# Performance work log

Hardware: AMD Instinct MI355X
Metric: run time of the kernel (lower is better)

Reference implementation:

```python
import jax, jax.numpy as jnp
import numpy as np

H = 64          # hidden_dim
I = 4           # input_dim
L = 4           # num_layers
O = 5           # output_dim
B = 256         # batch
T = 2048        # seq_len


def setup_inputs() -> dict:
    key = jax.random.key(0)
    ks = jax.random.split(key, 20)
    s = 1.0 / np.sqrt(H)  # PyTorch GRU init scale
    x = jax.random.normal(ks[0], (B, T, I), dtype=jnp.float32)
    # layer 0 input->hidden weights ([3H, I]); layers 1..3 input is H
    w_ih0 = jax.random.uniform(ks[1], (3 * H, I), jnp.float32, -s, s)
    w_ih_rest = jax.random.uniform(ks[2], (L - 1, 3 * H, H), jnp.float32, -s, s)
    w_hh = jax.random.uniform(ks[3], (L, 3 * H, H), jnp.float32, -s, s)
    b_ih = jax.random.uniform(ks[4], (L, 3 * H), jnp.float32, -s, s)
    b_hh = jax.random.uniform(ks[5], (L, 3 * H), jnp.float32, -s, s)
    fc_w = jax.random.uniform(ks[6], (O, H), jnp.float32, -s, s)
    fc_b = jax.random.uniform(ks[7], (O,), jnp.float32, -s, s)
    return {"x": x, "w_ih0": w_ih0, "w_ih_rest": w_ih_rest, "w_hh": w_hh,
            "b_ih": b_ih, "b_hh": b_hh, "fc_w": fc_w, "fc_b": fc_b}


def _gru_layer(x_seq, w_ih, w_hh, b_ih, b_hh):
    """x_seq: [B,T,Din] -> [B,T,H]. PyTorch GRU cell equations."""
    # Precompute all input-side gate projections in one GEMM: [B,T,3H]
    gx = jnp.einsum('btd,gd->btg', x_seq, w_ih) + b_ih
    gx = jnp.swapaxes(gx, 0, 1)  # [T,B,3H] for scan over time

    def step(h, gx_t):
        gh = h @ w_hh.T + b_hh                 # [B,3H]
        xr, xz, xn = jnp.split(gx_t, 3, axis=-1)
        hr, hz, hn = jnp.split(gh, 3, axis=-1)
        r = jax.nn.sigmoid(xr + hr)
        z = jax.nn.sigmoid(xz + hz)
        n = jnp.tanh(xn + r * hn)
        h_new = (1.0 - z) * n + z * h
        return h_new, h_new

    h0 = jnp.zeros((x_seq.shape[0], H), dtype=x_seq.dtype)
    _, hs = jax.lax.scan(step, h0, gx)
    return jnp.swapaxes(hs, 0, 1)  # [B,T,H]


def reference(x, w_ih0, w_ih_rest, w_hh, b_ih, b_hh, fc_w, fc_b):
    # 4 stacked GRU layers (dropout=0.3 between layers is a no-op in eval mode)
    out = _gru_layer(x, w_ih0, w_hh[0], b_ih[0], b_hh[0])
    for l in range(1, L):
        out = _gru_layer(out, w_ih_rest[l - 1], w_hh[l], b_ih[l], b_hh[l])
    # final linear head on last timestep: [B,O]
    return out[:, -1, :] @ fc_w.T + fc_b
```

## Files before the change

kernel.cpp:

```cpp
#include <hip/hip_runtime.h>

#define T_LEN 2048
#define NTHREADS 896

__global__ __launch_bounds__(NTHREADS)
__attribute__((amdgpu_waves_per_eu(4, 4)))
void gru_fused(const float* __restrict__ x,
               const float* __restrict__ w_ih0,
               const float* __restrict__ w_ih_rest,
               const float* __restrict__ w_hh,
               const float* __restrict__ b_ih,
               const float* __restrict__ b_hh,
               const float* __restrict__ fc_w,
               const float* __restrict__ fc_b,
               float* __restrict__ out)
{
    extern __shared__ float smem[];
    float* xs   = smem;
    float* hst  = xs + 8192;
    float* gbuf = hst + 256;
    float* w0s  = gbuf + 1344;
    float* bihs = w0s + 768;
    float* bhhs = bihs + 768;

    const int tid = threadIdx.x;
    const int b   = blockIdx.x;

    {
        const float4* xg = (const float4*)(x + (size_t)b * (T_LEN * 4));
        float4* xd = (float4*)xs;
        for (int i = tid; i < T_LEN; i += NTHREADS) xd[i] = xg[i];
    }
    if (tid < 192)                    ((float4*)w0s)[tid]        = ((const float4*)w_ih0)[tid];
    else if (tid < 384)               ((float4*)bihs)[tid - 192] = ((const float4*)b_ih)[tid - 192];
    else if (tid < 576)               ((float4*)bhhs)[tid - 384] = ((const float4*)b_hh)[tid - 384];
    if (tid < 256) hst[tid] = 0.0f;

    const int g2   = tid >> 7;
    const int r7   = tid & 127;
    const int c    = r7 >> 1;
    const int half = r7 & 1;
    const int src  = (g2 < 3) ? g2 : (g2 - 3);

    float4 w4[3][8];
    {
        const float* wsrc = (g2 < 3) ? (w_ih_rest + g2 * (192 * 64))
                                     : (w_hh      + (g2 - 3) * (192 * 64));
        #pragma unroll
        for (int i = 0; i < 3; ++i) {
            const float4* p = (const float4*)(wsrc + (i * 64 + c) * 64 + half * 32);
            #pragma unroll
            for (int q = 0; q < 8; ++q) w4[i][q] = p[q];
        }
    }

    const int cl = tid >> 6;
    const int cc = tid & 63;
    __syncthreads();

    const float4* vb4 = (const float4*)(hst + src * 64 + half * 32);

    for (int s = 0; s < T_LEN + 3; ++s) {
        float a0 = 0.f, a1 = 0.f, a2 = 0.f;
        #pragma unroll
        for (int q = 0; q < 8; ++q) {
            const float4 f = vb4[q];
            a0 = fmaf(f.x, w4[0][q].x, a0); a0 = fmaf(f.y, w4[0][q].y, a0);
            a0 = fmaf(f.z, w4[0][q].z, a0); a0 = fmaf(f.w, w4[0][q].w, a0);
            a1 = fmaf(f.x, w4[1][q].x, a1); a1 = fmaf(f.y, w4[1][q].y, a1);
            a1 = fmaf(f.z, w4[1][q].z, a1); a1 = fmaf(f.w, w4[1][q].w, a1);
            a2 = fmaf(f.x, w4[2][q].x, a2); a2 = fmaf(f.y, w4[2][q].y, a2);
            a2 = fmaf(f.z, w4[2][q].z, a2); a2 = fmaf(f.w, w4[2][q].w, a2);
        }
        a0 += __shfl_xor(a0, 1);
        a1 += __shfl_xor(a1, 1);
        a2 += __shfl_xor(a2, 1);
        if (half == 0) {
            gbuf[g2 * 192 +       c] = a0;
            gbuf[g2 * 192 +  64 + c] = a1;
            gbuf[g2 * 192 + 128 + c] = a2;
        }
        __syncthreads();

        if (tid < 256) {
            const int t = s - cl;
            if (t >= 0 && t < T_LEN) {
                float xr, xz, xn;
                if (cl == 0) {
                    const float4 xv = ((const float4*)xs)[t];
                    const float4 u0 = ((const float4*)w0s)[cc];
                    const float4 u1 = ((const float4*)w0s)[64 + cc];
                    const float4 u2 = ((const float4*)w0s)[128 + cc];
                    xr = bihs[cc]       + xv.x * u0.x + xv.y * u0.y + xv.z * u0.z + xv.w * u0.w;
                    xz = bihs[64 + cc]  + xv.x * u1.x + xv.y * u1.y + xv.z * u1.z + xv.w * u1.w;
                    xn = bihs[128 + cc] + xv.x * u2.x + xv.y * u2.y + xv.z * u2.z + xv.w * u2.w;
                } else {
                    xr = bihs[cl * 192 +       cc] + gbuf[(cl - 1) * 192 +       cc];
                    xz = bihs[cl * 192 +  64 + cc] + gbuf[(cl - 1) * 192 +  64 + cc];
                    xn = bihs[cl * 192 + 128 + cc] + gbuf[(cl - 1) * 192 + 128 + cc];
                }
                const float hr = bhhs[cl * 192 +       cc] + gbuf[(3 + cl) * 192 +       cc];
                const float hz = bhhs[cl * 192 +  64 + cc] + gbuf[(3 + cl) * 192 +  64 + cc];
                const float hn = bhhs[cl * 192 + 128 + cc] + gbuf[(3 + cl) * 192 + 128 + cc];
                const float hold = hst[cl * 64 + cc];

                const float r = 1.0f / (1.0f + __expf(-(xr + hr)));
                const float z = 1.0f / (1.0f + __expf(-(xz + hz)));
                const float e = __expf(2.0f * (xn + r * hn));
                const float n = 1.0f - 2.0f / (e + 1.0f);
                hst[cl * 64 + cc] = n + z * (hold - n);
            }
        }
        __syncthreads();
    }

    if (tid < 5) {
        float acc = fc_b[tid];
        const float* wf = fc_w + tid * 64;
        #pragma unroll
        for (int k = 0; k < 64; ++k) acc = fmaf(hst[3 * 64 + k], wf[k], acc);
        out[(size_t)b * 5 + tid] = acc;
    }
}

extern "C" void kernel_launch(void* const* d_in, const int* in_sizes, int n_in,
                              void* d_out, int out_size, void* d_ws, size_t ws_size,
                              hipStream_t stream) {
    const float* x         = (const float*)d_in[0];
    const float* w_ih0     = (const float*)d_in[1];
    const float* w_ih_rest = (const float*)d_in[2];
    const float* w_hh      = (const float*)d_in[3];
    const float* b_ih      = (const float*)d_in[4];
    const float* b_hh      = (const float*)d_in[5];
    const float* fc_w      = (const float*)d_in[6];
    const float* fc_b      = (const float*)d_in[7];

    const size_t lds_bytes = (8192 + 256 + 1344 + 768 + 768 + 768) * sizeof(float);
    gru_fused<<<dim3(256), dim3(NTHREADS), lds_bytes, stream>>>(
        x, w_ih0, w_ih_rest, w_hh, b_ih, b_hh, fc_w, fc_b, (float*)d_out);
}
```

Before: 1.967 ms.

## Halve block size so each thread owns full 64-wide dot products

Each thread now holds the full 64-element weight rows for its three gate outputs in registers (192 VGPRs of weights) instead of splitting each row across two lanes. This removes the cross-lane shuffle reduction and the half-lane predicated store, and halves the block to 448 threads (7 waves) at 2 waves per EU. In exchange each thread's serial FMA chain per step doubles and register pressure rises sharply; an empty asm barrier pins the weights in VGPRs to keep the compiler from spilling or rematerialising them.

```diff
diff --git a/kernel.cpp b/kernel.cpp
--- a/kernel.cpp
+++ b/kernel.cpp
@@ -1,10 +1,10 @@
 #include <hip/hip_runtime.h>
 
 #define T_LEN 2048
-#define NTHREADS 896
+#define NTHREADS 448
 
 __global__ __launch_bounds__(NTHREADS)
-__attribute__((amdgpu_waves_per_eu(4, 4)))
+__attribute__((amdgpu_waves_per_eu(2, 2)))
 void gru_fused(const float* __restrict__ x,
                const float* __restrict__ w_ih0,
                const float* __restrict__ w_ih_rest,
@@ -31,39 +31,43 @@
         float4* xd = (float4*)xs;
         for (int i = tid; i < T_LEN; i += NTHREADS) xd[i] = xg[i];
     }
-    if (tid < 192)                    ((float4*)w0s)[tid]        = ((const float4*)w_ih0)[tid];
-    else if (tid < 384)               ((float4*)bihs)[tid - 192] = ((const float4*)b_ih)[tid - 192];
-    else if (tid < 576)               ((float4*)bhhs)[tid - 384] = ((const float4*)b_hh)[tid - 384];
+    for (int i = tid; i < 192; i += NTHREADS) ((float4*)w0s)[i]  = ((const float4*)w_ih0)[i];
+    for (int i = tid; i < 192; i += NTHREADS) ((float4*)bihs)[i] = ((const float4*)b_ih)[i];
+    for (int i = tid; i < 192; i += NTHREADS) ((float4*)bhhs)[i] = ((const float4*)b_hh)[i];
     if (tid < 256) hst[tid] = 0.0f;
 
-    const int g2   = tid >> 7;
-    const int r7   = tid & 127;
-    const int c    = r7 >> 1;
-    const int half = r7 & 1;
-    const int src  = (g2 < 3) ? g2 : (g2 - 3);
+    const int g = tid >> 6;
+    const int c = tid & 63;
+    const int src = (g < 3) ? g : (g - 3);
 
-    float4 w4[3][8];
+    float4 w4[3][16];
     {
-        const float* wsrc = (g2 < 3) ? (w_ih_rest + g2 * (192 * 64))
-                                     : (w_hh      + (g2 - 3) * (192 * 64));
+        const float* wsrc = (g < 3) ? (w_ih_rest + g * (192 * 64))
+                                    : (w_hh      + (g - 3) * (192 * 64));
         #pragma unroll
         for (int i = 0; i < 3; ++i) {
-            const float4* p = (const float4*)(wsrc + (i * 64 + c) * 64 + half * 32);
+            const float4* p = (const float4*)(wsrc + (i * 64 + c) * 64);
             #pragma unroll
-            for (int q = 0; q < 8; ++q) w4[i][q] = p[q];
+            for (int q = 0; q < 16; ++q) w4[i][q] = p[q];
         }
     }
+    #pragma unroll
+    for (int i = 0; i < 3; ++i)
+        #pragma unroll
+        for (int q = 0; q < 16; ++q)
+            asm volatile("" : "+v"(w4[i][q].x), "+v"(w4[i][q].y),
+                             "+v"(w4[i][q].z), "+v"(w4[i][q].w));
 
     const int cl = tid >> 6;
     const int cc = tid & 63;
     __syncthreads();
 
-    const float4* vb4 = (const float4*)(hst + src * 64 + half * 32);
+    const float4* vb4 = (const float4*)(hst + src * 64);
 
     for (int s = 0; s < T_LEN + 3; ++s) {
         float a0 = 0.f, a1 = 0.f, a2 = 0.f;
         #pragma unroll
-        for (int q = 0; q < 8; ++q) {
+        for (int q = 0; q < 16; ++q) {
             const float4 f = vb4[q];
             a0 = fmaf(f.x, w4[0][q].x, a0); a0 = fmaf(f.y, w4[0][q].y, a0);
             a0 = fmaf(f.z, w4[0][q].z, a0); a0 = fmaf(f.w, w4[0][q].w, a0);
@@ -72,14 +76,9 @@
             a2 = fmaf(f.x, w4[2][q].x, a2); a2 = fmaf(f.y, w4[2][q].y, a2);
             a2 = fmaf(f.z, w4[2][q].z, a2); a2 = fmaf(f.w, w4[2][q].w, a2);
         }
-        a0 += __shfl_xor(a0, 1);
-        a1 += __shfl_xor(a1, 1);
-        a2 += __shfl_xor(a2, 1);
-        if (half == 0) {
-            gbuf[g2 * 192 +       c] = a0;
-            gbuf[g2 * 192 +  64 + c] = a1;
-            gbuf[g2 * 192 + 128 + c] = a2;
-        }
+        gbuf[g * 192 +       c] = a0;
+        gbuf[g * 192 +  64 + c] = a1;
+        gbuf[g * 192 + 128 + c] = a2;
         __syncthreads();
 
         if (tid < 256) {
```

After: 2.151 ms. +9.4%, slower.
